# Kernel tuning notes

Hardware: AMD Instinct MI355X
Metric: run time of the kernel (lower is better)

Reference implementation:

```python
import jax, jax.numpy as jnp
import numpy as np

B, S, HID = 2, 4096, 3584
NH, NKV, HD, FD = 16, 8, 256, 64
CHUNK = 64

def _rope_tables(seq_len, dim, base=10000.0):
    inv = 1.0 / (base ** (np.arange(0, dim, 2) / dim))      # [dim/2]
    f = np.outer(np.arange(seq_len), inv)                   # [S, dim/2]
    return jnp.asarray(np.cos(f), jnp.float32), jnp.asarray(np.sin(f), jnp.float32)

def setup_inputs() -> dict:
    key = jax.random.key(0)
    ks = jax.random.split(key, 8)
    def w(k, shape, fan):
        return jax.random.normal(k, shape, jnp.float32) * (fan ** -0.5)
    cos, sin = _rope_tables(S, HD)
    return dict(
        hidden_states=jax.random.normal(ks[0], (B, S, HID), jnp.float32),
        cos=cos, sin=sin,
        Wq=w(ks[1], (HID, NH * HD), HID),
        Wk=w(ks[2], (HID, NKV * HD), HID),
        Wv=w(ks[3], (HID, NKV * HD), HID),
        Wo=w(ks[4], (NH * HD, HID), NH * HD),
        fmq=w(ks[5], (NH, HD, FD), HD),
        fmk=w(ks[6], (NH, HD, FD), HD),
    )

def apply_rope(x, cos, sin):
    # Gemma split-half rotary. x: [B,S,h,D]; cos/sin: [S,D/2]
    d2 = x.shape[-1] // 2
    x1, x2 = x[..., :d2], x[..., d2:]
    c = cos[None, :, None, :]
    s = sin[None, :, None, :]
    return jnp.concatenate([x1 * c - x2 * s, x1 * s + x2 * c], axis=-1)

def feature_map(x, w):
    # Hedgehog: per-head linear then cat(softmax(z), softmax(-z)).
    # x: [B,h,S,D], w: [h,D,F] -> [B,h,S,2F]
    z = jnp.einsum('bhsd,hdf->bhsf', x, w)
    return jnp.concatenate([jax.nn.softmax(z, axis=-1), jax.nn.softmax(-z, axis=-1)], axis=-1)

def chunk_linear_attn(q, k, v, chunk=CHUNK):
    # q,k: [B,H,T,dk]; v: [B,H,T,dv]; T divisible by chunk (S=4096, chunk=64)
    b, h, T, dk = q.shape
    dv = v.shape[-1]
    n = T // chunk
    q = q.reshape(b, h, n, chunk, dk) * (dk ** -0.5)
    k = k.reshape(b, h, n, chunk, dk)
    v = v.reshape(b, h, n, chunk, dv)
    kv = jnp.einsum('bhncd,bhnce->bhnde', k, v)          # per-chunk K^T V: [b,h,n,dk,dv]
    kv = jnp.cumsum(kv, axis=2)
    kv = jnp.concatenate([jnp.zeros_like(kv[:, :, :1]), kv[:, :, :-1]], axis=2)  # exclusive
    inter = jnp.einsum('bhncd,bhnde->bhnce', q, kv)
    scores = jnp.einsum('bhncd,bhnkd->bhnck', q, k)
    causal = jnp.tril(jnp.ones((chunk, chunk), dtype=bool))
    scores = jnp.where(causal, scores, jnp.zeros((), scores.dtype))
    intra = jnp.einsum('bhnck,bhnke->bhnce', scores, v)
    return (inter + intra).reshape(b, h, T, dv)

def reference(hidden_states, cos, sin, Wq, Wk, Wv, Wo, fmq, fmk):
    b, s, _ = hidden_states.shape
    q = (hidden_states @ Wq).reshape(b, s, NH, HD)
    k = (hidden_states @ Wk).reshape(b, s, NKV, HD)
    v = (hidden_states @ Wv).reshape(b, s, NKV, HD)
    q = apply_rope(q, cos, sin)
    k = apply_rope(k, cos, sin)
    g = NH // NKV
    k = jnp.repeat(k, g, axis=2)   # GQA expansion
    v = jnp.repeat(v, g, axis=2)
    q = q.transpose(0, 2, 1, 3)    # [B,H,S,D]
    k = k.transpose(0, 2, 1, 3)
    v = v.transpose(0, 2, 1, 3)
    q = feature_map(q, fmq)        # [B,H,S,2F]
    k = feature_map(k, fmk)
    o = chunk_linear_attn(q, k, v)                      # [B,H,S,HD]
    o = o.transpose(0, 2, 1, 3).reshape(b, s, NH * HD)
    return o @ Wo
```

## Files before the change

kernel.cpp:

```cpp
#include <hip/hip_runtime.h>

typedef float  f32x4  __attribute__((ext_vector_type(4)));
typedef __bf16 bf16x4 __attribute__((ext_vector_type(4)));
typedef __bf16 bf16x8 __attribute__((ext_vector_type(8)));

#define MFMA16(a,b,c) __builtin_amdgcn_mfma_f32_16x16x32_bf16((a),(b),(c),0,0,0)

__device__ __forceinline__ void async_copy16(void* lds, const void* gmem) {
  __builtin_amdgcn_global_load_lds(
      (const __attribute__((address_space(1))) void*)gmem,
      (__attribute__((address_space(3))) void*)lds, 16, 0, 0);
}

template<int N> __device__ __forceinline__ void vmcnt_gate() {
  if constexpr (N == 8) asm volatile("s_waitcnt vmcnt(8)" ::: "memory");
  else if constexpr (N == 6) asm volatile("s_waitcnt vmcnt(6)" ::: "memory");
  else if constexpr (N == 4) asm volatile("s_waitcnt vmcnt(4)" ::: "memory");
  else if constexpr (N == 2) asm volatile("s_waitcnt vmcnt(2)" ::: "memory");
  else if constexpr (N == 0) asm volatile("s_waitcnt vmcnt(0)" ::: "memory");
  __builtin_amdgcn_sched_barrier(0);
}

#define LGKM(N) do { __builtin_amdgcn_sched_barrier(0); \
                     asm volatile("s_waitcnt lgkmcnt(" #N ")" ::: "memory"); \
                     __builtin_amdgcn_sched_barrier(0); } while (0)

#define BARRIER do { __builtin_amdgcn_sched_barrier(0); \
                     __builtin_amdgcn_s_barrier(); \
                     __builtin_amdgcn_sched_barrier(0); } while (0)

__global__ __launch_bounds__(256) void convert_kernel(const float* __restrict__ in,
                                                      __bf16* __restrict__ out, size_t n4) {
  size_t i = (size_t)blockIdx.x * 256 + threadIdx.x;
  if (i >= n4) return;
  f32x4 v = *(const f32x4*)(in + i * 4);
  bf16x4 o;
  #pragma unroll
  for (int j = 0; j < 4; ++j) o[j] = (__bf16)v[j];
  *(bf16x4*)(out + i * 4) = o;
}

__global__ __launch_bounds__(256) void transpose_kernel(const float* __restrict__ in,
                                                        __bf16* __restrict__ out, int R, int C) {
  __shared__ float tile[32][33];
  int bx = blockIdx.x, by = blockIdx.y;
  int tx = threadIdx.x & 31, ty0 = threadIdx.x >> 5;
  #pragma unroll
  for (int i = 0; i < 4; ++i) {
    int r = by * 32 + ty0 + i * 8;
    tile[ty0 + i * 8][tx] = in[(size_t)r * C + bx * 32 + tx];
  }
  __syncthreads();
  #pragma unroll
  for (int i = 0; i < 4; ++i) {
    int c = bx * 32 + ty0 + i * 8;
    out[(size_t)c * R + by * 32 + tx] = (__bf16)tile[tx][ty0 + i * 8];
  }
}


template<bool REMAP>
__device__ __forceinline__ void stage_q(__bf16* region, int qrow, const __bf16* src,
                                        int K, int w, int l) {
  int s = qrow + w * 8 + (l >> 3);
  int gr = REMAP ? (((s >> 5) << 4) | (s & 15) | (((s >> 4) & 1) << 7)) : s;
  async_copy16(region + (size_t)(qrow + w * 8) * 64,
               src + (size_t)gr * K + (((l & 7) ^ (s & 7)) << 3));
}

template<bool LATE, bool EARLY, bool NEXT, int G2, int G3, bool BMAP>
__device__ __forceinline__ void tile_body(__bf16* smem,
                                          const __bf16* Apan, const __bf16* Bpan,
                                          int K, int tau, int wm, int wn,
                                          int lo, int hi, int w, int l,
                                          bf16x8 (&aA)[4], bf16x8 (&aB)[4],
                                          bf16x8 (&bA)[4], bf16x8 (&bB)[4],
                                          f32x4 (&acc)[8][4]) {
  const int buf = tau & 1;
  __bf16* Ab = smem + buf * 32768;
  __bf16* Bb = Ab + 16384;
  __bf16* An = smem + (buf ^ 1) * 32768;
  __bf16* Bn = An + 16384;

  #pragma unroll
  for (int t = 0; t < 4; ++t) {
    int ra = wm * 128 + 64 + t * 16 + lo;
    aB[t] = *(const bf16x8*)(Ab + (size_t)ra * 64 + ((hi ^ (ra & 7)) << 3));
  }
  if constexpr (LATE) {
    const __bf16* Ap1 = Apan + (size_t)(tau + 1) * 64;
    stage_q<false>(An, 64,  Ap1, K, w, l);
    stage_q<false>(An, 192, Ap1, K, w, l);
  }
  LGKM(4);
  __builtin_amdgcn_s_setprio(1);
  #pragma unroll
  for (int mt = 0; mt < 4; ++mt)
    #pragma unroll
    for (int nt = 0; nt < 4; ++nt)
      acc[mt][nt] = MFMA16(aA[mt], bA[nt], acc[mt][nt]);
  __builtin_amdgcn_s_setprio(0);
  BARRIER;

  #pragma unroll
  for (int t = 0; t < 4; ++t) {
    int ra = wm * 128 + t * 16 + lo;
    aA[t] = *(const bf16x8*)(Ab + (size_t)ra * 64 + (((4 + hi) ^ (ra & 7)) << 3));
  }
  #pragma unroll
  for (int t = 0; t < 4; ++t) {
    int rb = wn * 64 + t * 16 + lo;
    bB[t] = *(const bf16x8*)(Bb + (size_t)rb * 64 + (((4 + hi) ^ (rb & 7)) << 3));
  }
  LGKM(8);
  __builtin_amdgcn_s_setprio(1);
  #pragma unroll
  for (int mt = 0; mt < 4; ++mt)
    #pragma unroll
    for (int nt = 0; nt < 4; ++nt)
      acc[4 + mt][nt] = MFMA16(aB[mt], bA[nt], acc[4 + mt][nt]);
  __builtin_amdgcn_s_setprio(0);
  BARRIER;

  #pragma unroll
  for (int t = 0; t < 4; ++t) {
    int ra = wm * 128 + 64 + t * 16 + lo;
    aB[t] = *(const bf16x8*)(Ab + (size_t)ra * 64 + (((4 + hi) ^ (ra & 7)) << 3));
  }
  LGKM(4);
  __builtin_amdgcn_s_setprio(1);
  #pragma unroll
  for (int mt = 0; mt < 4; ++mt)
    #pragma unroll
    for (int nt = 0; nt < 4; ++nt)
      acc[mt][nt] = MFMA16(aA[mt], bB[nt], acc[mt][nt]);
  __builtin_amdgcn_s_setprio(0);
  if constexpr (G2 >= 0) vmcnt_gate<G2>();
  BARRIER;

  if constexpr (NEXT) {
    #pragma unroll
    for (int t = 0; t < 4; ++t) {
      int ra = wm * 128 + t * 16 + lo;
      aA[t] = *(const bf16x8*)(An + (size_t)ra * 64 + ((hi ^ (ra & 7)) << 3));
    }
    #pragma unroll
    for (int t = 0; t < 4; ++t) {
      int rb = wn * 64 + t * 16 + lo;
      bA[t] = *(const bf16x8*)(Bn + (size_t)rb * 64 + ((hi ^ (rb & 7)) << 3));
    }
  }
  if constexpr (EARLY) {
    const __bf16* Ap2 = Apan + (size_t)(tau + 2) * 64;
    const __bf16* Bp2 = Bpan + (size_t)(tau + 2) * 64;
    stage_q<false>(Ab, 0,   Ap2, K, w, l);
    stage_q<false>(Ab, 128, Ap2, K, w, l);
    stage_q<BMAP>(Bb, 0,   Bp2, K, w, l);
    stage_q<BMAP>(Bb, 64,  Bp2, K, w, l);
    stage_q<BMAP>(Bb, 128, Bp2, K, w, l);
    stage_q<BMAP>(Bb, 192, Bp2, K, w, l);
  }
  if constexpr (NEXT) LGKM(8); else LGKM(0);
  __builtin_amdgcn_s_setprio(1);
  #pragma unroll
  for (int mt = 0; mt < 4; ++mt)
    #pragma unroll
    for (int nt = 0; nt < 4; ++nt)
      acc[4 + mt][nt] = MFMA16(aB[mt], bB[nt], acc[4 + mt][nt]);
  __builtin_amdgcn_s_setprio(0);
  if constexpr (G3 >= 0) vmcnt_gate<G3>();
  BARRIER;
}

template <typename CT, int MODE>
__global__ __launch_bounds__(512, 2) void gemm256_kernel(const __bf16* __restrict__ A,
                                                         const __bf16* __restrict__ Bt,
                                                         CT* __restrict__ C, int M, int N, int K,
                                                         const float* __restrict__ cosT,
                                                         const float* __restrict__ sinT,
                                                         int Hh) {
  extern __shared__ __bf16 smem[];
  constexpr bool BMAP = (MODE == 1);

  const int gx = gridDim.x;
  const int nwg = gx * gridDim.y;
  const int wg = blockIdx.y * gx + blockIdx.x;
  const int qq = nwg >> 3;
  const int id2 = (wg & 7) * qq + (wg >> 3);
  const int m0 = (id2 / gx) * 256, n0 = (id2 % gx) * 256;

  const int tid = threadIdx.x;
  const int l = tid & 63, w = tid >> 6;
  const int lo = l & 15, hi = l >> 4;
  const int wm = w >> 2, wn = w & 3;

  const __bf16* Apan = A + (size_t)m0 * K;
  const __bf16* Bpan = Bt + (size_t)n0 * K;

  f32x4 acc[8][4] = {};
  bf16x8 aA[4], aB[4], bA[4], bB[4];

  stage_q<false>(smem,          0,   Apan, K, w, l);
  stage_q<false>(smem,          128, Apan, K, w, l);
  stage_q<BMAP>(smem + 16384,  0,   Bpan, K, w, l);
  stage_q<BMAP>(smem + 16384,  64,  Bpan, K, w, l);
  stage_q<BMAP>(smem + 16384,  128, Bpan, K, w, l);
  stage_q<BMAP>(smem + 16384,  192, Bpan, K, w, l);
  stage_q<false>(smem,          64,  Apan, K, w, l);
  stage_q<false>(smem,          192, Apan, K, w, l);
  stage_q<false>(smem + 32768,  0,   Apan + 64, K, w, l);
  stage_q<false>(smem + 32768,  128, Apan + 64, K, w, l);
  stage_q<BMAP>(smem + 49152,  0,   Bpan + 64, K, w, l);
  stage_q<BMAP>(smem + 49152,  64,  Bpan + 64, K, w, l);
  stage_q<BMAP>(smem + 49152,  128, Bpan + 64, K, w, l);
  stage_q<BMAP>(smem + 49152,  192, Bpan + 64, K, w, l);
  stage_q<false>(smem + 32768,  64,  Apan + 64, K, w, l);
  stage_q<false>(smem + 32768,  192, Apan + 64, K, w, l);
  vmcnt_gate<8>();
  BARRIER;

  #pragma unroll
  for (int t = 0; t < 4; ++t) {
    int ra = wm * 128 + t * 16 + lo;
    aA[t] = *(const bf16x8*)(smem + (size_t)ra * 64 + ((hi ^ (ra & 7)) << 3));
  }
  #pragma unroll
  for (int t = 0; t < 4; ++t) {
    int rb = wn * 64 + t * 16 + lo;
    bA[t] = *(const bf16x8*)(smem + 16384 + (size_t)rb * 64 + ((hi ^ (rb & 7)) << 3));
  }

  const int T = K >> 6;
  tile_body<false, true,  true,  2,  6, BMAP>(smem, Apan, Bpan, K, 0,     wm, wn, lo, hi, w, l, aA, aB, bA, bB, acc);
  for (int tau = 1; tau < T - 2; ++tau)
    tile_body<true, true,  true,  2,  6, BMAP>(smem, Apan, Bpan, K, tau,   wm, wn, lo, hi, w, l, aA, aB, bA, bB, acc);
  tile_body<true,  false, true,  2,  0, BMAP>(smem, Apan, Bpan, K, T - 2, wm, wn, lo, hi, w, l, aA, aB, bA, bB, acc);
  tile_body<false, false, false, -1, -1, BMAP>(smem, Apan, Bpan, K, T - 1, wm, wn, lo, hi, w, l, aA, aB, bA, bB, acc);

  if constexpr (MODE == 0) {
    #pragma unroll
    for (int mt = 0; mt < 8; ++mt)
      #pragma unroll
      for (int nt = 0; nt < 4; ++nt) {
        int col = n0 + wn * 64 + nt * 16 + lo;
        #pragma unroll
        for (int r = 0; r < 4; ++r) {
          int row = m0 + wm * 128 + mt * 16 + 4 * hi + r;
          C[(size_t)row * N + col] = (CT)acc[mt][nt][r];
        }
      }
  } else if constexpr (MODE == 2) {
    const int kv = n0 >> 8;
    #pragma unroll
    for (int mt = 0; mt < 8; ++mt)
      #pragma unroll
      for (int nt = 0; nt < 4; ++nt) {
        int col = wn * 64 + nt * 16 + lo;
        #pragma unroll
        for (int r = 0; r < 4; ++r) {
          int row = m0 + wm * 128 + mt * 16 + 4 * hi + r;
          int bb = row >> 12, sdx = row & 4095;
          C[(((size_t)(bb * Hh + kv)) * 4096 + sdx) * 256 + col] = (CT)acc[mt][nt][r];
        }
      }
  } else {
    const int hq = n0 >> 8;
    #pragma unroll
    for (int mt = 0; mt < 8; ++mt)
      #pragma unroll
      for (int ntp = 0; ntp < 4; ntp += 2) {
        int d = (2 * wn + (ntp >> 1)) * 16 + lo;
        #pragma unroll
        for (int r = 0; r < 4; ++r) {
          int row = m0 + wm * 128 + mt * 16 + 4 * hi + r;
          int bb = row >> 12, sdx = row & 4095;
          float cc = cosT[(size_t)sdx * 128 + d];
          float ss = sinT[(size_t)sdx * 128 + d];
          float x1 = acc[mt][ntp][r], x2 = acc[mt][ntp + 1][r];
          size_t base = (((size_t)(bb * Hh + hq)) * 4096 + sdx) * 256;
          C[base + d]       = (CT)(x1 * cc - x2 * ss);
          C[base + d + 128] = (CT)(x1 * ss + x2 * cc);
        }
      }
  }
}

__global__ __launch_bounds__(256) void fm_kernel(const __bf16* __restrict__ rope,
                                                 const float* __restrict__ fm,
                                                 __bf16* __restrict__ out, int srcH, float scale) {
  __shared__ __bf16 fmT[64][256];
  int bh = blockIdx.y;
  int h = bh & 15, b = bh >> 4;
  int s0 = blockIdx.x * 128;
  int tid = threadIdx.x, lane = tid & 63, wid = tid >> 6, hi = lane >> 4, lo = lane & 15;

  const float* fmh = fm + (size_t)h * 256 * 64;
  for (int i = tid; i < 256 * 64; i += 256) {
    int d = i >> 6, f = i & 63;
    fmT[f][(((d >> 3) ^ (f & 7)) << 3) | (d & 7)] = (__bf16)fmh[i];
  }
  __syncthreads();

  int srch = (srcH == 16) ? h : (h >> 1);
  const __bf16* abase = rope + ((size_t)(b * srcH + srch) * 4096 + s0 + 32 * wid) * 256;
  f32x4 acc[2][4] = {};
  for (int kk = 0; kk < 256; kk += 32) {
    bf16x8 a[2], bf[4];
    #pragma unroll
    for (int mt = 0; mt < 2; ++mt)
      a[mt] = *(const bf16x8*)(abase + (size_t)(16 * mt + lo) * 256 + kk + 8 * hi);
    const int G = (kk >> 3) + hi;
    #pragma unroll
    for (int nt = 0; nt < 4; ++nt) {
      int f = 16 * nt + lo;
      bf[nt] = *(const bf16x8*)&fmT[f][(G ^ (f & 7)) << 3];
    }
    #pragma unroll
    for (int mt = 0; mt < 2; ++mt)
      #pragma unroll
      for (int nt = 0; nt < 4; ++nt)
        acc[mt][nt] = MFMA16(a[mt], bf[nt], acc[mt][nt]);
  }

  size_t obase = ((size_t)(b * 16 + h) * 4096 + s0 + 32 * wid);
  #pragma unroll
  for (int mt = 0; mt < 2; ++mt) {
    #pragma unroll
    for (int r = 0; r < 4; ++r) {
      float z0 = acc[mt][0][r], z1 = acc[mt][1][r], z2 = acc[mt][2][r], z3 = acc[mt][3][r];
      float mx = fmaxf(fmaxf(z0, z1), fmaxf(z2, z3));
      float mn = fminf(fminf(z0, z1), fminf(z2, z3));
      #pragma unroll
      for (int off = 1; off < 16; off <<= 1) {
        mx = fmaxf(mx, __shfl_xor(mx, off));
        mn = fminf(mn, __shfl_xor(mn, off));
      }
      float ep0 = __expf(z0 - mx), ep1 = __expf(z1 - mx), ep2 = __expf(z2 - mx), ep3 = __expf(z3 - mx);
      float en0 = __expf(mn - z0), en1 = __expf(mn - z1), en2 = __expf(mn - z2), en3 = __expf(mn - z3);
      float sp = ep0 + ep1 + ep2 + ep3, sn = en0 + en1 + en2 + en3;
      #pragma unroll
      for (int off = 1; off < 16; off <<= 1) {
        sp += __shfl_xor(sp, off);
        sn += __shfl_xor(sn, off);
      }
      float rp = scale / sp, rn = scale / sn;
      int row = 16 * mt + 4 * hi + r;
      __bf16* op = out + (obase + row) * 128;
      op[0  + lo] = (__bf16)(ep0 * rp);  op[16 + lo] = (__bf16)(ep1 * rp);
      op[32 + lo] = (__bf16)(ep2 * rp);  op[48 + lo] = (__bf16)(ep3 * rp);
      op[64 + lo] = (__bf16)(en0 * rn);  op[80 + lo] = (__bf16)(en1 * rn);
      op[96 + lo] = (__bf16)(en2 * rn);  op[112 + lo] = (__bf16)(en3 * rn);
    }
  }
}

__global__ __launch_bounds__(256) void attn_kernel(const __bf16* __restrict__ qf,
                                                   const __bf16* __restrict__ kf,
                                                   const __bf16* __restrict__ vp,
                                                   __bf16* __restrict__ o) {
  __shared__ __bf16 k_s[64][128];
  __shared__ __bf16 vT_s[32][64];
  __shared__ __bf16 sc_s[64][64];
  __shared__ __bf16 STb[32][128];

  int bid = blockIdx.x;
  int g   = ((bid >> 6) << 3) | (bid & 7);
  int dvb = (bid >> 3) & 7;
  int h = g & 15, b = g >> 4;
  int dv0 = dvb * 32;
  int tid = threadIdx.x, lane = tid & 63, wid = tid >> 6, hi = lane >> 4, lo = lane & 15;

  const __bf16* qh = qf + ((size_t)(b * 16 + h)) * 4096 * 128;
  const __bf16* kh = kf + ((size_t)(b * 16 + h)) * 4096 * 128;
  const __bf16* vh = vp + ((size_t)(b * 8 + (h >> 1))) * 4096 * 256 + dv0;
  __bf16* oh = o + ((size_t)b * 4096) * 4096 + h * 256 + dv0;

  {
    unsigned int* z = (unsigned int*)&STb[0][0];
    for (int i = tid; i < 2048; i += 256) z[i] = 0u;
  }
  f32x4 st[2][2] = {};

  for (int n = 0; n < 64; ++n) {
    int s0 = n * 64;
    #pragma unroll
    for (int i = 0; i < 4; ++i) {
      int rb = (wid * 4 + i) * 4;
      int r = rb + (lane >> 4);
      int Glog = (lane & 15) ^ (r & 7);
      async_copy16(&k_s[rb][0], kh + (size_t)(s0 + r) * 128 + Glog * 8);
    }
    {
      int c = tid >> 2, d8 = (tid & 3) * 8;
      bf16x8 vv = *(const bf16x8*)(vh + (size_t)(s0 + c) * 256 + d8);
      #pragma unroll
      for (int j = 0; j < 8; ++j) {
        int dv = d8 + j;
        vT_s[dv][(((c >> 3) ^ (dv & 7)) << 3) | (c & 7)] = vv[j];
      }
    }
    __syncthreads();

    bf16x8 aq[4];
    #pragma unroll
    for (int kq = 0; kq < 4; ++kq)
      aq[kq] = *(const bf16x8*)(qh + (size_t)(s0 + 16 * wid + lo) * 128 + 32 * kq + 8 * hi);

    f32x4 acc_o[2] = {}, sacc[4] = {};
    #pragma unroll
    for (int nt = 0; nt < 2; ++nt)
      #pragma unroll
      for (int kq = 0; kq < 4; ++kq) {
        int rr = 16 * nt + lo, G = 4 * kq + hi;
        bf16x8 bf = *(const bf16x8*)&STb[rr][(G ^ (rr & 7)) << 3];
        acc_o[nt] = MFMA16(aq[kq], bf, acc_o[nt]);
      }
    #pragma unroll
    for (int nt = 0; nt < 4; ++nt)
      #pragma unroll
      for (int kq = 0; kq < 4; ++kq) {
        int rr = 16 * nt + lo, G = 4 * kq + hi;
        bf16x8 bf = *(const bf16x8*)&k_s[rr][(G ^ (rr & 7)) << 3];
        sacc[nt] = MFMA16(aq[kq], bf, sacc[nt]);
      }
    #pragma unroll
    for (int nt = 0; nt < 4; ++nt)
      #pragma unroll
      for (int r = 0; r < 4; ++r) {
        int c = 16 * wid + 4 * hi + r;
        int cp = 16 * nt + lo;
        float v = (cp <= c) ? sacc[nt][r] : 0.0f;
        sc_s[c][(((cp >> 3) ^ (c & 7)) << 3) | (cp & 7)] = (__bf16)v;
      }
    asm volatile("" ::: "memory");
    #pragma unroll
    for (int nt = 0; nt < 2; ++nt)
      #pragma unroll
      for (int kq = 0; kq < 2; ++kq) {
        int rA = 16 * wid + lo, GA = 4 * kq + hi;
        bf16x8 af = *(const bf16x8*)&sc_s[rA][(GA ^ (rA & 7)) << 3];
        int rB = 16 * nt + lo;
        bf16x8 bf = *(const bf16x8*)&vT_s[rB][(GA ^ (rB & 7)) << 3];
        acc_o[nt] = MFMA16(af, bf, acc_o[nt]);
      }
    #pragma unroll
    for (int nt = 0; nt < 2; ++nt)
      #pragma unroll
      for (int r = 0; r < 4; ++r) {
        int c = 16 * wid + 4 * hi + r;
        oh[(size_t)(s0 + c) * 4096 + 16 * nt + lo] = (__bf16)acc_o[nt][r];
      }
    __syncthreads();

    bf16x8 bu[2][2];
    #pragma unroll
    for (int q = 0; q < 2; ++q) {
      int dk = 16 * (2 * wid + q) + lo;
      #pragma unroll
      for (int kq = 0; kq < 2; ++kq) {
        bf16x8 tmp;
        #pragma unroll
        for (int j = 0; j < 8; ++j) {
          int c = 32 * kq + 8 * hi + j;
          tmp[j] = k_s[c][(((dk >> 3) ^ (c & 7)) << 3) | (dk & 7)];
        }
        bu[q][kq] = tmp;
      }
    }
    #pragma unroll
    for (int mt = 0; mt < 2; ++mt)
      #pragma unroll
      for (int kq = 0; kq < 2; ++kq) {
        int rA = 16 * mt + lo, GA = 4 * kq + hi;
        bf16x8 av = *(const bf16x8*)&vT_s[rA][(GA ^ (rA & 7)) << 3];
        #pragma unroll
        for (int q = 0; q < 2; ++q)
          st[mt][q] = MFMA16(av, bu[q][kq], st[mt][q]);
      }
    #pragma unroll
    for (int mt = 0; mt < 2; ++mt)
      #pragma unroll
      for (int q = 0; q < 2; ++q) {
        int dk = 16 * (2 * wid + q) + lo;
        #pragma unroll
        for (int r = 0; r < 4; ++r) {
          int dvr = 16 * mt + 4 * hi + r;
          STb[dvr][(((dk >> 3) ^ (dvr & 7)) << 3) | (dk & 7)] = (__bf16)st[mt][q][r];
        }
      }
    __syncthreads();
  }
}

extern "C" void kernel_launch(void* const* d_in, const int* in_sizes, int n_in,
                              void* d_out, int out_size, void* d_ws, size_t ws_size,
                              hipStream_t stream) {
  (void)in_sizes; (void)n_in; (void)out_size; (void)ws_size;
  const float* hs   = (const float*)d_in[0];
  const float* cosT = (const float*)d_in[1];
  const float* sinT = (const float*)d_in[2];
  const float* Wq   = (const float*)d_in[3];
  const float* Wk   = (const float*)d_in[4];
  const float* Wv   = (const float*)d_in[5];
  const float* Wo   = (const float*)d_in[6];
  const float* fmq  = (const float*)d_in[7];
  const float* fmk  = (const float*)d_in[8];
  float* out = (float*)d_out;
  char* ws = (char*)d_ws;

  hipFuncSetAttribute((const void*)gemm256_kernel<float, 0>,
                      hipFuncAttributeMaxDynamicSharedMemorySize, 131072);
  hipFuncSetAttribute((const void*)gemm256_kernel<__bf16, 1>,
                      hipFuncAttributeMaxDynamicSharedMemorySize, 131072);
  hipFuncSetAttribute((const void*)gemm256_kernel<__bf16, 2>,
                      hipFuncAttributeMaxDynamicSharedMemorySize, 131072);

  const size_t MB = 1024ull * 1024ull;
  __bf16* Xb   = (__bf16*)(ws + 0);
  __bf16* qfb  = (__bf16*)(ws + 0);
  __bf16* kfb  = (__bf16*)(ws + 34 * MB);
  __bf16* Wqt  = (__bf16*)(ws + 70 * MB);
  __bf16* ob   = (__bf16*)(ws + 70 * MB);
  __bf16* Wkt  = (__bf16*)(ws + 104 * MB);
  __bf16* Wvt  = (__bf16*)(ws + 119 * MB);
  __bf16* Wot  = (__bf16*)(ws + 140 * MB);
  __bf16* ropq = (__bf16*)(ws + 170 * MB);
  __bf16* ropk = (__bf16*)(ws + 238 * MB);
  __bf16* vpb  = (__bf16*)(ws + 272 * MB);

  convert_kernel<<<28672, 256, 0, stream>>>(hs, Xb, (size_t)8192 * 3584 / 4);
  transpose_kernel<<<dim3(128, 112), 256, 0, stream>>>(Wq, Wqt, 3584, 4096);
  transpose_kernel<<<dim3(64, 112),  256, 0, stream>>>(Wk, Wkt, 3584, 2048);
  transpose_kernel<<<dim3(64, 112),  256, 0, stream>>>(Wv, Wvt, 3584, 2048);
  transpose_kernel<<<dim3(112, 128), 256, 0, stream>>>(Wo, Wot, 4096, 3584);

  gemm256_kernel<__bf16, 1><<<dim3(16, 32), 512, 131072, stream>>>(
      Xb, Wqt, ropq, 8192, 4096, 3584, cosT, sinT, 16);
  gemm256_kernel<__bf16, 1><<<dim3(8, 32),  512, 131072, stream>>>(
      Xb, Wkt, ropk, 8192, 2048, 3584, cosT, sinT, 8);
  gemm256_kernel<__bf16, 2><<<dim3(8, 32),  512, 131072, stream>>>(
      Xb, Wvt, vpb, 8192, 2048, 3584, nullptr, nullptr, 8);

  fm_kernel<<<dim3(32, 32), 256, 0, stream>>>(ropq, fmq, qfb, 16, 0.08838834764831845f);
  fm_kernel<<<dim3(32, 32), 256, 0, stream>>>(ropk, fmk, kfb, 8, 1.0f);

  attn_kernel<<<256, 256, 0, stream>>>(qfb, kfb, vpb, ob);

  gemm256_kernel<float, 0><<<dim3(14, 32), 512, 131072, stream>>>(
      ob, Wot, out, 8192, 3584, 4096, nullptr, nullptr, 0);
}
```

Measured before the change: 944.3 us.

## Double-buffer K/V tiles and prefetch next chunk's Q/K/V in attention kernel

Converts the chunked linear-attention kernel to a two-stage pipeline. K and transposed V shared-memory tiles are double-buffered, and the next chunk's K (async copy to LDS), V and Q (register loads) are issued at the top of each iteration so global latency overlaps the current chunk's MFMA work. The last iteration skips the unneeded state update, and one barrier per iteration is replaced by the macro-based wait+barrier. This doubles K/V LDS usage and raises register pressure from the prefetched Q and V fragments, which may reduce occupancy.

Result: no change. 930.2 us, median of 3 (-1.5%).

```diff
diff --git a/kernel.cpp b/kernel.cpp
--- a/kernel.cpp
+++ b/kernel.cpp
@@ -358,8 +358,8 @@
                                                    const __bf16* __restrict__ kf,
                                                    const __bf16* __restrict__ vp,
                                                    __bf16* __restrict__ o) {
-  __shared__ __bf16 k_s[64][128];
-  __shared__ __bf16 vT_s[32][64];
+  __shared__ __bf16 k_s[2][64][128];
+  __shared__ __bf16 vT_s[2][32][64];
   __shared__ __bf16 sc_s[64][64];
   __shared__ __bf16 STb[32][128];
 
@@ -381,30 +381,55 @@
   }
   f32x4 st[2][2] = {};
 
+  const int vc = tid >> 2, vd8 = (tid & 3) * 8;
+  bf16x8 aqN[4], aqC[4], vvN;
+
+  #pragma unroll
+  for (int i = 0; i < 4; ++i) {
+    int rb = (wid * 4 + i) * 4;
+    int r = rb + (lane >> 4);
+    int Glog = (lane & 15) ^ (r & 7);
+    async_copy16(&k_s[0][rb][0], kh + (size_t)r * 128 + Glog * 8);
+  }
+  __builtin_amdgcn_sched_barrier(0);
+  vvN = *(const bf16x8*)(vh + (size_t)vc * 256 + vd8);
+  __builtin_amdgcn_sched_barrier(0);
+  #pragma unroll
+  for (int kq = 0; kq < 4; ++kq)
+    aqN[kq] = *(const bf16x8*)(qh + (size_t)(16 * wid + lo) * 128 + 32 * kq + 8 * hi);
+  __builtin_amdgcn_sched_barrier(0);
+  #pragma unroll
+  for (int j = 0; j < 8; ++j) {
+    int dv = vd8 + j;
+    vT_s[0][dv][(((vc >> 3) ^ (dv & 7)) << 3) | (vc & 7)] = vvN[j];
+  }
+  LGKM(0);
+  BARRIER;
+
   for (int n = 0; n < 64; ++n) {
-    int s0 = n * 64;
-    #pragma unroll
-    for (int i = 0; i < 4; ++i) {
-      int rb = (wid * 4 + i) * 4;
-      int r = rb + (lane >> 4);
-      int Glog = (lane & 15) ^ (r & 7);
-      async_copy16(&k_s[rb][0], kh + (size_t)(s0 + r) * 128 + Glog * 8);
-    }
-    {
-      int c = tid >> 2, d8 = (tid & 3) * 8;
-      bf16x8 vv = *(const bf16x8*)(vh + (size_t)(s0 + c) * 256 + d8);
-      #pragma unroll
-      for (int j = 0; j < 8; ++j) {
-        int dv = d8 + j;
-        vT_s[dv][(((c >> 3) ^ (dv & 7)) << 3) | (c & 7)] = vv[j];
-      }
-    }
-    __syncthreads();
-
-    bf16x8 aq[4];
-    #pragma unroll
-    for (int kq = 0; kq < 4; ++kq)
-      aq[kq] = *(const bf16x8*)(qh + (size_t)(s0 + 16 * wid + lo) * 128 + 32 * kq + 8 * hi);
+    const int buf = n & 1;
+    const int s0 = n * 64;
+
+    #pragma unroll
+    for (int kq = 0; kq < 4; ++kq) aqC[kq] = aqN[kq];
+
+    if (n < 63) {
+      const int s1 = s0 + 64;
+      #pragma unroll
+      for (int i = 0; i < 4; ++i) {
+        int rb = (wid * 4 + i) * 4;
+        int r = rb + (lane >> 4);
+        int Glog = (lane & 15) ^ (r & 7);
+        async_copy16(&k_s[buf ^ 1][rb][0], kh + (size_t)(s1 + r) * 128 + Glog * 8);
+      }
+      __builtin_amdgcn_sched_barrier(0);
+      vvN = *(const bf16x8*)(vh + (size_t)(s1 + vc) * 256 + vd8);
+      __builtin_amdgcn_sched_barrier(0);
+      #pragma unroll
+      for (int kq = 0; kq < 4; ++kq)
+        aqN[kq] = *(const bf16x8*)(qh + (size_t)(s1 + 16 * wid + lo) * 128 + 32 * kq + 8 * hi);
+      __builtin_amdgcn_sched_barrier(0);
+    }
 
     f32x4 acc_o[2] = {}, sacc[4] = {};
     #pragma unroll
@@ -413,15 +438,15 @@
       for (int kq = 0; kq < 4; ++kq) {
         int rr = 16 * nt + lo, G = 4 * kq + hi;
         bf16x8 bf = *(const bf16x8*)&STb[rr][(G ^ (rr & 7)) << 3];
-        acc_o[nt] = MFMA16(aq[kq], bf, acc_o[nt]);
+        acc_o[nt] = MFMA16(aqC[kq], bf, acc_o[nt]);
       }
     #pragma unroll
     for (int nt = 0; nt < 4; ++nt)
       #pragma unroll
       for (int kq = 0; kq < 4; ++kq) {
         int rr = 16 * nt + lo, G = 4 * kq + hi;
-        bf16x8 bf = *(const bf16x8*)&k_s[rr][(G ^ (rr & 7)) << 3];
-        sacc[nt] = MFMA16(aq[kq], bf, sacc[nt]);
+        bf16x8 bf = *(const bf16x8*)&k_s[buf][rr][(G ^ (rr & 7)) << 3];
+        sacc[nt] = MFMA16(aqC[kq], bf, sacc[nt]);
       }
     #pragma unroll
     for (int nt = 0; nt < 4; ++nt)
@@ -440,7 +465,7 @@
         int rA = 16 * wid + lo, GA = 4 * kq + hi;
         bf16x8 af = *(const bf16x8*)&sc_s[rA][(GA ^ (rA & 7)) << 3];
         int rB = 16 * nt + lo;
-        bf16x8 bf = *(const bf16x8*)&vT_s[rB][(GA ^ (rB & 7)) << 3];
+        bf16x8 bf = *(const bf16x8*)&vT_s[buf][rB][(GA ^ (rB & 7)) << 3];
         acc_o[nt] = MFMA16(af, bf, acc_o[nt]);
       }
     #pragma unroll
@@ -450,7 +475,10 @@
         int c = 16 * wid + 4 * hi + r;
         oh[(size_t)(s0 + c) * 4096 + 16 * nt + lo] = (__bf16)acc_o[nt][r];
       }
-    __syncthreads();
+
+    if (n == 63) break;
+
+    BARRIER;
 
     bf16x8 bu[2][2];
     #pragma unroll
@@ -462,7 +490,7 @@
         #pragma unroll
         for (int j = 0; j < 8; ++j) {
           int c = 32 * kq + 8 * hi + j;
-          tmp[j] = k_s[c][(((dk >> 3) ^ (c & 7)) << 3) | (dk & 7)];
+          tmp[j] = k_s[buf][c][(((dk >> 3) ^ (c & 7)) << 3) | (dk & 7)];
         }
         bu[q][kq] = tmp;
       }
@@ -472,7 +500,7 @@
       #pragma unroll
       for (int kq = 0; kq < 2; ++kq) {
         int rA = 16 * mt + lo, GA = 4 * kq + hi;
-        bf16x8 av = *(const bf16x8*)&vT_s[rA][(GA ^ (rA & 7)) << 3];
+        bf16x8 av = *(const bf16x8*)&vT_s[buf][rA][(GA ^ (rA & 7)) << 3];
         #pragma unroll
         for (int q = 0; q < 2; ++q)
           st[mt][q] = MFMA16(av, bu[q][kq], st[mt][q]);
@@ -488,7 +516,13 @@
           STb[dvr][(((dk >> 3) ^ (dvr & 7)) << 3) | (dk & 7)] = (__bf16)st[mt][q][r];
         }
       }
-    __syncthreads();
+    #pragma unroll
+    for (int j = 0; j < 8; ++j) {
+      int dv = vd8 + j;
+      vT_s[buf ^ 1][dv][(((vc >> 3) ^ (dv & 7)) << 3) | (vc & 7)] = vvN[j];
+    }
+    LGKM(0);
+    BARRIER;
   }
 }
 
```
